# Performance work log

Hardware: AMD Instinct MI355X
Metric: run time of the kernel (lower is better)

Reference implementation:

```python
import jax, jax.numpy as jnp
import numpy as np

B, D, E = 128, 1024, 1024   # batch, word_rnn_size, word_encoding_size
NV, NL = 36, 20             # visual regions, language memory slots
T = 4                       # max_att_step
EPS = 0.01                  # opt.epsilon
SCALE = 0.02


def _lstm_cell(x, h, c, Wih, Whh, bih, bhh):
    # torch.nn.LSTMCell gate order: i, f, g, o
    g = x @ Wih.T + bih + h @ Whh.T + bhh
    i, f, gg, o = jnp.split(g, 4, axis=-1)
    c2 = jax.nn.sigmoid(f) * c + jax.nn.sigmoid(i) * jnp.tanh(gg)
    h2 = jax.nn.sigmoid(o) * jnp.tanh(c2)
    return h2, c2


def _kv_attention(h_att, vkey, vval, lkey, lval, kvs):
    # stand-in for the externally-passed kv_attention module:
    # scaled dot-product attention over visual and language memories
    q = h_att + kvs                                   # [B,D]
    inv = 1.0 / np.sqrt(D)
    va = jax.nn.softmax(jnp.einsum('bnd,bd->bn', vkey, q) * inv, axis=-1)
    vctx = jnp.einsum('bn,bnd->bd', va, vval)
    la = jax.nn.softmax(jnp.einsum('bmd,bd->bm', lkey, q) * inv, axis=-1)
    lctx = jnp.einsum('bm,bmd->bd', la, lval)
    return vctx, lctx, jnp.tanh(kvs + vctx + lctx)


def _update_kv(out, vkey, lkey):
    # stand-in for the externally-passed update_kv module
    return vkey + 0.01 * out[:, None, :], lkey + 0.01 * out[:, None, :]


def _forward(xt, fc_feats, visual_value, visual_key, lang_value, lang_key,
             kv_state, state_h, state_c,
             att_Wih, att_Whh, att_bih, att_bhh,
             lang_Wih, lang_Whh, lang_bih, lang_bhh,
             conf_W1, conf_b1, conf_W2, conf_b2,
             it, max_att_step):
    word_exist = (it > 0).astype(jnp.float32)         # [B]
    prev_h = state_h[-1]
    # att_lstm input is constant across halting steps (state is not updated in the loop)
    att_in = jnp.concatenate([prev_h, fc_feats, xt], axis=1)  # [B, E+2D]
    z1 = jnp.zeros((B, 1), jnp.float32)
    zD = jnp.zeros((B, D), jnp.float32)
    zB = jnp.zeros((B,), jnp.float32)
    carry0 = (z1, jnp.ones((B, 1), jnp.float32), zD, zD, zD, zD, zD, zB,
              visual_key, lang_key, kv_state)

    def body(carry, i):
        accum, sel, hA, cA, hL, cL, outA, cost, vkey, lkey, kvs = carry
        h_att, c_att = _lstm_cell(att_in, state_h[0], state_c[0],
                                  att_Wih, att_Whh, att_bih, att_bhh)
        vctx, lctx, kvs = _kv_attention(h_att, vkey, visual_value, lkey, lang_value, kvs)
        lang_in = jnp.concatenate([vctx, lctx, h_att], axis=1)  # [B,3D]
        h_lang, c_lang = _lstm_cell(lang_in, state_h[1], state_c[1],
                                    lang_Wih, lang_Whh, lang_bih, lang_bhh)
        out = h_lang  # F.dropout in eval mode is identity
        vkey, lkey = _update_kv(out, vkey, lkey)
        # confidence MLP: Linear -> ReLU -> Linear -> Sigmoid
        p = jax.nn.sigmoid(jax.nn.relu(h_lang @ conf_W1.T + conf_b1) @ conf_W2.T + conf_b2)  # [B,1]
        beta = p * (1.0 - accum)
        accum = accum + beta * sel
        hA = hA + beta * h_att * sel
        cA = cA + beta * c_att * sel
        hL = hL + beta * h_lang * sel
        cL = cL + beta * c_lang * sel
        outA = outA + beta * out * sel
        cost = cost + (i + 1.0) * (1.0 - p[:, 0]) * sel[:, 0]
        sel = jax.lax.stop_gradient((accum < 1.0 - EPS).astype(jnp.float32)) * sel
        return (accum, sel, hA, cA, hL, cL, outA, cost, vkey, lkey, kvs), None

    carry, _ = jax.lax.scan(body, carry0, jnp.arange(max_att_step, dtype=jnp.float32))
    accum, sel, hA, cA, hL, cL, outA, cost, vkey, lkey, kvs = carry
    hA = hA / accum
    cA = cA / accum
    hL = hL / accum
    cL = cL / accum
    outA = outA / accum
    new_h = jnp.stack([hA, hL])
    new_c = jnp.stack([cA, cL])
    return outA, vkey, lkey, cost * word_exist, new_h, new_c, kvs


def setup_inputs() -> dict:
    ks = jax.random.split(jax.random.key(0), 20)
    n = lambda k, s, sc=1.0: jax.random.normal(k, s, dtype=jnp.float32) * sc
    return {
        'xt': n(ks[0], (B, E)),
        'it': jax.random.randint(ks[1], (B,), 0, 9487, dtype=jnp.int32),
        'fc_feats': n(ks[2], (B, D)),
        'visual_value': n(ks[3], (B, NV, D)),
        'visual_key': n(ks[4], (B, NV, D)),
        'lang_value': n(ks[5], (B, NL, D)),
        'lang_key': n(ks[6], (B, NL, D)),
        'kv_state': n(ks[7], (B, D)),
        'state_h': n(ks[8], (2, B, D)),
        'state_c': n(ks[9], (2, B, D)),
        'max_att_step': T,
        'att_Wih': n(ks[10], (4 * D, E + 2 * D), SCALE),
        'att_Whh': n(ks[11], (4 * D, D), SCALE),
        'att_bih': jnp.zeros((4 * D,), jnp.float32),
        'att_bhh': jnp.zeros((4 * D,), jnp.float32),
        'lang_Wih': n(ks[12], (4 * D, 3 * D), SCALE),
        'lang_Whh': n(ks[13], (4 * D, D), SCALE),
        'lang_bih': jnp.zeros((4 * D,), jnp.float32),
        'lang_bhh': jnp.zeros((4 * D,), jnp.float32),
        'conf_W1': n(ks[14], (D, D), SCALE),
        'conf_b1': jnp.zeros((D,), jnp.float32),
        'conf_W2': n(ks[15], (1, D), SCALE),
        'conf_b2': jnp.zeros((1,), jnp.float32),
    }


def reference(xt, it, fc_feats, visual_value, visual_key, lang_value, lang_key,
              kv_state, state_h, state_c, max_att_step,
              att_Wih, att_Whh, att_bih, att_bhh,
              lang_Wih, lang_Whh, lang_bih, lang_bhh,
              conf_W1, conf_b1, conf_W2, conf_b2):
    return _forward(xt, fc_feats, visual_value, visual_key, lang_value, lang_key,
                    kv_state, state_h, state_c,
                    att_Wih, att_Whh, att_bih, att_bhh,
                    lang_Wih, lang_Whh, lang_bih, lang_bhh,
                    conf_W1, conf_b1, conf_W2, conf_b2,
                    it, max_att_step)
```

## Files before the change

### kernel.cpp

```cpp
#include <hip/hip_runtime.h>
#include <hip/hip_bf16.h>

constexpr int B  = 128;
constexpr int D  = 1024;
constexpr int NV = 36;
constexpr int NL = 20;
constexpr int BD = B * D;
constexpr float EPS = 0.01f;
constexpr int NSLOT = 16;

constexpr long SL  = 524288;
constexpr long SLB = 2097152;
constexpr long SLC = 524288;
constexpr long OFF_GPA   = 0;
constexpr long OFF_GPLB  = OFF_GPA + 16 * SL;
constexpr long OFF_LBASE = OFF_GPLB + 8 * SL;
constexpr long OFF_GPB   = OFF_LBASE + SL;
constexpr long OFF_GPC   = OFF_GPB + 4 * SLB;
constexpr long OFF_HATT2 = OFF_GPC + 4 * SLC;
constexpr long OFF_HLB   = OFF_HATT2 + BD;
constexpr long OFF_CLB   = OFF_HLB + 524288;
constexpr long OFF_S2    = OFF_CLB + 524288;
constexpr long OFF_VVB   = OFF_S2 + BD;
constexpr long OFF_LVB   = OFF_VVB + 2359296;
constexpr long OFF_VKB   = OFF_LVB + 1310720;
constexpr long OFF_LKB   = OFF_VKB + 2359296;
constexpr long OFF_HATB  = OFF_LKB + 1310720;
constexpr long OFF_SH1B  = OFF_HATB + 65536;
constexpr long OFF_VCXB  = OFF_SH1B + 65536;
constexpr long OFF_LCXB  = OFF_VCXB + 262144;

typedef float f32x4 __attribute__((ext_vector_type(4)));
typedef short s16x8 __attribute__((ext_vector_type(8)));

__device__ __forceinline__ float sigf(float x) { return 1.f / (1.f + expf(-x)); }

__device__ __forceinline__ short f2bf(float f) {
  __hip_bfloat16 h = __float2bfloat16(f);
  return *reinterpret_cast<short*>(&h);
}
__device__ __forceinline__ float bf2f(short s) {
  unsigned u = ((unsigned)(unsigned short)s) << 16;
  return __uint_as_float(u);
}

__device__ __forceinline__ f32x4 LD4(const float* p) { return *(const f32x4*)p; }
__device__ __forceinline__ void ST4(float* p, f32x4 v) { *(f32x4*)p = v; }

__device__ __forceinline__ void conv_bf16(const float* __restrict__ src,
                                          __hip_bfloat16* __restrict__ dst,
                                          long nelem) {
  const long total = nelem >> 2;
  for (long i = (long)blockIdx.x * 256 + threadIdx.x; i < total;
       i += (long)gridDim.x * 256) {
    f32x4 v = LD4(src + i * 4);
    *(short4*)((short*)dst + i * 4) =
        short4{f2bf(v[0]), f2bf(v[1]), f2bf(v[2]), f2bf(v[3])};
  }
}

__global__ __launch_bounds__(256) void conv_kv(
    const float* __restrict__ vkey, const float* __restrict__ lkey,
    const float* __restrict__ vval, const float* __restrict__ lval,
    const float* __restrict__ sh1,
    __hip_bfloat16* __restrict__ vkb, __hip_bfloat16* __restrict__ lkb,
    __hip_bfloat16* __restrict__ vvb, __hip_bfloat16* __restrict__ lvb,
    __hip_bfloat16* __restrict__ sh1b) {
  conv_bf16(vkey, vkb, (long)B * NV * 1024);
  conv_bf16(lkey, lkb, (long)B * NL * 1024);
  conv_bf16(vval, vvb, (long)B * NV * 1024);
  conv_bf16(lval, lvb, (long)B * NL * 1024);
  conv_bf16(sh1, sh1b, (long)BD);
}

struct GemmArgs {
  const void* A[NSLOT];
  const float* W[NSLOT];
  long wstride[NSLOT];
  int abf16[NSLOT];
  int klen;
};

__global__ __launch_bounds__(512, 4) void gemm_mfma(GemmArgs ga, int N,
                                                    long pstride,
                                                    float* __restrict__ gpart) {
  __shared__ __align__(16) short As[2][128][72];
  __shared__ __align__(16) short Bs[2][128][72];
  const int z = blockIdx.z;
  const int ab = ga.abf16[z];
  const float* __restrict__ Af = (const float*)ga.A[z];
  const short* __restrict__ Ah = (const short*)ga.A[z];
  const float* __restrict__ W = ga.W[z];
  const long wstr = ga.wstride[z];
  const int brow = blockIdx.y * 128;
  const int bcol = blockIdx.x * 128;
  float* __restrict__ out = gpart + (long)z * pstride;

  const int tid = threadIdx.x;
  const int wave = tid >> 6, lane = tid & 63;
  const int wr = wave >> 2, wc = wave & 3;
  const int lrow = lane & 15;
  const int lk8  = (lane >> 4) * 8;

  f32x4 acc[4][2];
#pragma unroll
  for (int m = 0; m < 4; ++m)
#pragma unroll
    for (int n = 0; n < 2; ++n) acc[m][n] = (f32x4){0.f, 0.f, 0.f, 0.f};

  float4 ra[4], rw[4];
  s16x8 rab[2];
#define LOAD_TILE(KT)                                                          \
  {                                                                            \
    const int kb = (KT) * 64;                                                  \
    if (ab) {                                                                  \
      _Pragma("unroll") for (int i = 0; i < 2; ++i) {                          \
        const int idx = tid + i * 512;                                         \
        const int r = idx >> 3, c8 = (idx & 7) * 8;                            \
        rab[i] = *(const s16x8*)(Ah + (long)(brow + r) * 1024 + kb + c8);      \
      }                                                                        \
    } else {                                                                   \
      _Pragma("unroll") for (int i = 0; i < 4; ++i) {                          \
        const int idx = tid + i * 512;                                         \
        const int r = idx >> 4, c4 = (idx & 15) * 4;                           \
        ra[i] = *(const float4*)(Af + (long)(brow + r) * 1024 + kb + c4);      \
      }                                                                        \
    }                                                                          \
    _Pragma("unroll") for (int i = 0; i < 4; ++i) {                            \
      const int idx = tid + i * 512;                                           \
      const int r = idx >> 4, c4 = (idx & 15) * 4;                             \
      rw[i] = *(const float4*)(W + (long)(bcol + r) * wstr + kb + c4);         \
    }                                                                          \
  }
#define WRITE_TILE(BUF)                                                        \
  {                                                                            \
    if (ab) {                                                                  \
      _Pragma("unroll") for (int i = 0; i < 2; ++i) {                          \
        const int idx = tid + i * 512;                                         \
        const int r = idx >> 3, c8 = (idx & 7) * 8;                            \
        *(s16x8*)(&As[BUF][r][c8]) = rab[i];                                   \
      }                                                                        \
    } else {                                                                   \
      _Pragma("unroll") for (int i = 0; i < 4; ++i) {                          \
        const int idx = tid + i * 512;                                         \
        const int r = idx >> 4, c4 = (idx & 15) * 4;                           \
        *(short4*)(&As[BUF][r][c4]) =                                          \
            short4{f2bf(ra[i].x), f2bf(ra[i].y), f2bf(ra[i].z), f2bf(ra[i].w)};\
      }                                                                        \
    }                                                                          \
    _Pragma("unroll") for (int i = 0; i < 4; ++i) {                            \
      const int idx = tid + i * 512;                                           \
      const int r = idx >> 4, c4 = (idx & 15) * 4;                             \
      *(short4*)(&Bs[BUF][r][c4]) =                                            \
          short4{f2bf(rw[i].x), f2bf(rw[i].y), f2bf(rw[i].z), f2bf(rw[i].w)};  \
    }                                                                          \
  }

  const int ntiles = ga.klen / 64;
  LOAD_TILE(0);
  WRITE_TILE(0);
  __syncthreads();
  for (int kt = 0; kt < ntiles; ++kt) {
    const int cur = kt & 1;
    const bool more = (kt + 1 < ntiles);
    if (more) LOAD_TILE(kt + 1);
#pragma unroll
    for (int kk = 0; kk < 64; kk += 32) {
      s16x8 af[4], bf[2];
#pragma unroll
      for (int m = 0; m < 4; ++m)
        af[m] = *(const s16x8*)(&As[cur][wr * 64 + m * 16 + lrow][kk + lk8]);
#pragma unroll
      for (int n = 0; n < 2; ++n)
        bf[n] = *(const s16x8*)(&Bs[cur][wc * 32 + n * 16 + lrow][kk + lk8]);
#pragma unroll
      for (int m = 0; m < 4; ++m)
#pragma unroll
        for (int n = 0; n < 2; ++n)
          acc[m][n] = __builtin_amdgcn_mfma_f32_16x16x32_bf16(
              af[m], bf[n], acc[m][n], 0, 0, 0);
    }
    if (more) WRITE_TILE(1 - cur);
    __syncthreads();
  }
#undef LOAD_TILE
#undef WRITE_TILE

#pragma unroll
  for (int m = 0; m < 4; ++m) {
#pragma unroll
    for (int n = 0; n < 2; ++n) {
      const int col = bcol + wc * 32 + n * 16 + lrow;
#pragma unroll
      for (int r = 0; r < 4; ++r) {
        const int row = brow + wr * 64 + m * 16 + (lane >> 4) * 4 + r;
        out[(long)row * N + col] = acc[m][n][r];
      }
    }
  }
}

constexpr long O1 = BD;
constexpr long O2 = O1 + (long)B * NV * D;
constexpr long O3 = O2 + (long)B * NL * D;
constexpr long O4 = O3 + B;
constexpr long O5 = O4 + 2L * BD;
constexpr long O6 = O5 + 2L * BD;
constexpr long O7 = O6 + BD;

__global__ __launch_bounds__(256) void lstm_att(
    const float* __restrict__ gp, const float* __restrict__ bih,
    const float* __restrict__ bhh, const float* __restrict__ c_prev,
    float* __restrict__ h, __hip_bfloat16* __restrict__ hb,
    float* __restrict__ out) {
  long idx = ((long)blockIdx.x * 256 + threadIdx.x) * 4;
  if (idx >= BD) return;
  int b = (int)(idx >> 10), d = (int)(idx & 1023);
  const long base = (long)b * 4096 + d;
  f32x4 g[4];
#pragma unroll
  for (int gi = 0; gi < 4; ++gi) {
    const long o = base + gi * 1024;
    f32x4 v = LD4(bih + gi * 1024 + d) + LD4(bhh + gi * 1024 + d);
#pragma unroll
    for (int s = 0; s < 16; ++s) v += LD4(gp + s * SL + o);
    g[gi] = v;
  }
  f32x4 cp = LD4(c_prev + idx), cc, hh;
#pragma unroll
  for (int j = 0; j < 4; ++j) {
    float ccj = sigf(g[1][j]) * cp[j] + sigf(g[0][j]) * tanhf(g[2][j]);
    cc[j] = ccj;
    hh[j] = sigf(g[3][j]) * tanhf(ccj);
  }
  ST4(h + idx, hh);
  *(short4*)((short*)hb + idx) =
      short4{f2bf(hh[0]), f2bf(hh[1]), f2bf(hh[2]), f2bf(hh[3])};
  ST4(out + O4 + idx, hh);
  ST4(out + O5 + idx, cc);
}

__global__ __launch_bounds__(256) void reduce8(
    const float* __restrict__ gp, const float* __restrict__ bih,
    const float* __restrict__ bhh, float* __restrict__ out) {
  long idx = ((long)blockIdx.x * 256 + threadIdx.x) * 4;
  if (idx >= (long)B * 4096) return;
  int col = (int)(idx & 4095);
  f32x4 v = LD4(bih + col) + LD4(bhh + col);
#pragma unroll
  for (int s = 0; s < 8; ++s) v += LD4(gp + s * SL + idx);
  ST4(out + idx, v);
}

__global__ __launch_bounds__(1024) void attn_mega(
    const float* __restrict__ h_att, const float* __restrict__ kv0,
    const __hip_bfloat16* __restrict__ vkb, const __hip_bfloat16* __restrict__ lkb,
    const __hip_bfloat16* __restrict__ vvb, const __hip_bfloat16* __restrict__ lvb,
    __hip_bfloat16* __restrict__ vctxB, __hip_bfloat16* __restrict__ lctxB,
    float* __restrict__ out_kvs) {
  const int b = blockIdx.x, tid = threadIdx.x;
  __shared__ short K[56][1024];
  __shared__ float q[1024];
  __shared__ float wgt[64];
  const int wave = tid >> 6, lane = tid & 63;

  for (int i = tid; i < 56 * 128; i += 1024) {
    const int r = i >> 7, c8 = (i & 127) * 8;
    const __hip_bfloat16* kp = (r < NV)
        ? vkb + ((long)b * NV + r) * 1024
        : lkb + ((long)b * NL + (r - NV)) * 1024;
    *(s16x8*)(&K[r][c8]) = *(const s16x8*)(kp + c8);
  }

  const float ha = h_att[(long)b * 1024 + tid];
  float kv = kv0[(long)b * 1024 + tid];

  for (int step = 0; step < 4; ++step) {
    q[tid] = ha + kv;
    __syncthreads();
    for (int n = wave; n < NV + NL; n += 16) {
      float s = 0.f;
#pragma unroll
      for (int j = 0; j < 2; ++j) {
        const int base = lane * 8 + j * 512;
        s16x8 k8 = *(const s16x8*)(&K[n][base]);
        f32x4 q0 = *(const f32x4*)(&q[base]);
        f32x4 q1 = *(const f32x4*)(&q[base + 4]);
#pragma unroll
        for (int e = 0; e < 4; ++e) {
          s += bf2f(k8[e]) * q0[e];
          s += bf2f(k8[e + 4]) * q1[e];
        }
      }
      for (int m = 32; m >= 1; m >>= 1) s += __shfl_xor(s, m);
      if (lane == 0) wgt[n] = s * (1.0f / 32.0f);
    }
    __syncthreads();
    if (wave == 0) {
      float x = (lane < NV) ? wgt[lane] : -1e30f;
      float m = x;
      for (int k = 32; k >= 1; k >>= 1) m = fmaxf(m, __shfl_xor(m, k));
      float e = (lane < NV) ? expf(x - m) : 0.f;
      float ssum = e;
      for (int k = 32; k >= 1; k >>= 1) ssum += __shfl_xor(ssum, k);
      if (lane < NV) wgt[lane] = e / ssum;
    } else if (wave == 1) {
      float x = (lane < NL) ? wgt[NV + lane] : -1e30f;
      float m = x;
      for (int k = 32; k >= 1; k >>= 1) m = fmaxf(m, __shfl_xor(m, k));
      float e = (lane < NL) ? expf(x - m) : 0.f;
      float ssum = e;
      for (int k = 32; k >= 1; k >>= 1) ssum += __shfl_xor(ssum, k);
      if (lane < NL) wgt[NV + lane] = e / ssum;
    }
    __syncthreads();
    const __hip_bfloat16* vb = vvb + (long)b * NV * 1024 + tid;
    float a0 = 0.f, a1 = 0.f, a2 = 0.f, a3 = 0.f;
#pragma unroll
    for (int n = 0; n < NV; n += 4) {
      a0 += __bfloat162float(vb[(long)(n + 0) * 1024]) * wgt[n + 0];
      a1 += __bfloat162float(vb[(long)(n + 1) * 1024]) * wgt[n + 1];
      a2 += __bfloat162float(vb[(long)(n + 2) * 1024]) * wgt[n + 2];
      a3 += __bfloat162float(vb[(long)(n + 3) * 1024]) * wgt[n + 3];
    }
    const float vc = (a0 + a1) + (a2 + a3);
    const __hip_bfloat16* lb = lvb + (long)b * NL * 1024 + tid;
    float c0 = 0.f, c1 = 0.f, c2 = 0.f, c3 = 0.f;
#pragma unroll
    for (int n = 0; n < NL; n += 4) {
      c0 += __bfloat162float(lb[(long)(n + 0) * 1024]) * wgt[NV + n + 0];
      c1 += __bfloat162float(lb[(long)(n + 1) * 1024]) * wgt[NV + n + 1];
      c2 += __bfloat162float(lb[(long)(n + 2) * 1024]) * wgt[NV + n + 2];
      c3 += __bfloat162float(lb[(long)(n + 3) * 1024]) * wgt[NV + n + 3];
    }
    const float lc = (c0 + c1) + (c2 + c3);
    const long orow = ((long)step * 128 + b) * 1024 + tid;
    vctxB[orow] = __float2bfloat16(vc);
    lctxB[orow] = __float2bfloat16(lc);
    kv = tanhf(kv + vc + lc);
    __syncthreads();
  }
  out_kvs[(long)b * 1024 + tid] = kv;
}

__global__ __launch_bounds__(256) void lstm_batch(
    const float* __restrict__ gpB, const float* __restrict__ lbase,
    const float* __restrict__ sc1, float* __restrict__ hB,
    float* __restrict__ cB) {
  long idx = ((long)blockIdx.x * 256 + threadIdx.x) * 4;
  if (idx >= 512L * 1024) return;
  const int row = (int)(idx >> 10);
  const int b = row & 127;
  const int d = (int)(idx & 1023);
  const long base = (long)row * 4096 + d;
  const long lbbase = (long)b * 4096 + d;
  f32x4 g[4];
#pragma unroll
  for (int gi = 0; gi < 4; ++gi) {
    const long o = gi * 1024;
    f32x4 v = LD4(lbase + lbbase + o);
#pragma unroll
    for (int s = 0; s < 4; ++s) v += LD4(gpB + s * SLB + base + o);
    g[gi] = v;
  }
  f32x4 cp = LD4(sc1 + (long)b * 1024 + d), cc, hh;
#pragma unroll
  for (int j = 0; j < 4; ++j) {
    float ccj = sigf(g[1][j]) * cp[j] + sigf(g[0][j]) * tanhf(g[2][j]);
    cc[j] = ccj;
    hh[j] = sigf(g[3][j]) * tanhf(ccj);
  }
  ST4(cB + idx, cc);
  ST4(hB + idx, hh);
}

__global__ __launch_bounds__(256) void halt_scan(
    const float* __restrict__ gpc, const float* __restrict__ cb1,
    const float* __restrict__ W2, const float* __restrict__ b2,
    const float* __restrict__ hB, const float* __restrict__ cB,
    const int* __restrict__ it, float* __restrict__ Sout,
    float* __restrict__ out) {
  const int b = blockIdx.x, tid = threadIdx.x;
  const int d0 = tid * 4;
  __shared__ float red[256];
  __shared__ float p_sh;
  const f32x4 w4 = LD4(W2 + d0);
  const f32x4 cb = LD4(cb1 + d0);
  f32x4 hl_acc = (f32x4){0.f, 0.f, 0.f, 0.f}, cl_acc = hl_acc, s_acc = hl_acc;
  float a = 0.f, sel = 1.f, cost = 0.f;

  for (int i = 0; i < 4; ++i) {
    const long o = ((long)i * 128 + b) * 1024 + d0;
    f32x4 rv = cb;
#pragma unroll
    for (int s = 0; s < 4; ++s) rv += LD4(gpc + s * SLC + o);
    float part = 0.f;
#pragma unroll
    for (int j = 0; j < 4; ++j) part += fmaxf(rv[j], 0.f) * w4[j];
    red[tid] = part;
    __syncthreads();
    for (int s = 128; s > 0; s >>= 1) {
      if (tid < s) red[tid] += red[tid + s];
      __syncthreads();
    }
    if (tid == 0) p_sh = sigf(red[0] + b2[0]);
    __syncthreads();
    const float p = p_sh;
    const float bs = p * (1.f - a) * sel;
    f32x4 hl = LD4(hB + o), cl = LD4(cB + o);
    hl_acc += hl * bs;
    cl_acc += cl * bs;
    s_acc += hl;
    cost += (float)(i + 1) * (1.f - p) * sel;
    a += bs;
    sel = (a < 1.f - EPS) ? sel : 0.f;
    __syncthreads();
  }
  const float inv_a = 1.f / a;
  const long ob = (long)b * 1024 + d0;
  ST4(out + ob, hl_acc * inv_a);
  ST4(out + O4 + BD + ob, hl_acc * inv_a);
  ST4(out + O5 + BD + ob, cl_acc * inv_a);
  ST4(Sout + ob, s_acc);
  if (tid == 0) out[O3 + b] = cost * ((it[b] > 0) ? 1.f : 0.f);
}

constexpr long VK = (long)B * NV * D;
constexpr long LK = (long)B * NL * D;

__global__ __launch_bounds__(256) void finalize2(
    const __hip_bfloat16* __restrict__ vkb, const __hip_bfloat16* __restrict__ lkb,
    const float* __restrict__ S, float* __restrict__ out) {
  long idx = ((long)blockIdx.x * 256 + threadIdx.x) * 8;
  if (idx < VK) {
    int b = (int)(idx / (NV * 1024));
    int d = (int)(idx & 1023);
    s16x8 k8 = *(const s16x8*)((const short*)vkb + idx);
    f32x4 s0 = LD4(S + (long)b * 1024 + d), s1 = LD4(S + (long)b * 1024 + d + 4);
    f32x4 o0, o1;
#pragma unroll
    for (int j = 0; j < 4; ++j) {
      o0[j] = bf2f(k8[j]) + 0.01f * s0[j];
      o1[j] = bf2f(k8[j + 4]) + 0.01f * s1[j];
    }
    ST4(out + O1 + idx, o0);
    ST4(out + O1 + idx + 4, o1);
  } else if (idx < VK + LK) {
    long r = idx - VK;
    int b = (int)(r / (NL * 1024));
    int d = (int)(r & 1023);
    s16x8 k8 = *(const s16x8*)((const short*)lkb + r);
    f32x4 s0 = LD4(S + (long)b * 1024 + d), s1 = LD4(S + (long)b * 1024 + d + 4);
    f32x4 o0, o1;
#pragma unroll
    for (int j = 0; j < 4; ++j) {
      o0[j] = bf2f(k8[j]) + 0.01f * s0[j];
      o1[j] = bf2f(k8[j + 4]) + 0.01f * s1[j];
    }
    ST4(out + O2 + r, o0);
    ST4(out + O2 + r + 4, o1);
  }
}

extern "C" void kernel_launch(void* const* d_in, const int* in_sizes, int n_in,
                              void* d_out, int out_size, void* d_ws, size_t ws_size,
                              hipStream_t stream) {
  const float* xt   = (const float*)d_in[0];
  const int*   it   = (const int*)d_in[1];
  const float* fc   = (const float*)d_in[2];
  const float* vval = (const float*)d_in[3];
  const float* vkey = (const float*)d_in[4];
  const float* lval = (const float*)d_in[5];
  const float* lkey = (const float*)d_in[6];
  const float* kv0  = (const float*)d_in[7];
  const float* sh   = (const float*)d_in[8];
  const float* sc   = (const float*)d_in[9];
  const float* aWih = (const float*)d_in[11];
  const float* aWhh = (const float*)d_in[12];
  const float* abih = (const float*)d_in[13];
  const float* abhh = (const float*)d_in[14];
  const float* lWih = (const float*)d_in[15];
  const float* lWhh = (const float*)d_in[16];
  const float* lbih = (const float*)d_in[17];
  const float* lbhh = (const float*)d_in[18];
  const float* cW1  = (const float*)d_in[19];
  const float* cb1  = (const float*)d_in[20];
  const float* cW2  = (const float*)d_in[21];
  const float* cb2  = (const float*)d_in[22];

  float* ws = (float*)d_ws;
  float* gpA   = ws + OFF_GPA;
  float* gpLB  = ws + OFF_GPLB;
  float* lbase = ws + OFF_LBASE;
  float* gpB   = ws + OFF_GPB;
  float* gpC   = ws + OFF_GPC;
  float* h_att = ws + OFF_HATT2;
  float* hB    = ws + OFF_HLB;
  float* cB    = ws + OFF_CLB;
  float* Sbuf  = ws + OFF_S2;
  __hip_bfloat16* vvb  = (__hip_bfloat16*)(ws + OFF_VVB);
  __hip_bfloat16* lvb  = (__hip_bfloat16*)(ws + OFF_LVB);
  __hip_bfloat16* vkb  = (__hip_bfloat16*)(ws + OFF_VKB);
  __hip_bfloat16* lkb  = (__hip_bfloat16*)(ws + OFF_LKB);
  __hip_bfloat16* hatb = (__hip_bfloat16*)(ws + OFF_HATB);
  __hip_bfloat16* sh1b = (__hip_bfloat16*)(ws + OFF_SH1B);
  __hip_bfloat16* vcxb = (__hip_bfloat16*)(ws + OFF_VCXB);
  __hip_bfloat16* lcxb = (__hip_bfloat16*)(ws + OFF_LCXB);

  const float* sh1 = sh + BD;
  const float* sc0 = sc;
  const float* sc1 = sc + BD;
  float* out = (float*)d_out;

  conv_kv<<<2048, 256, 0, stream>>>(vkey, lkey, vval, lval, sh1,
                                    vkb, lkb, vvb, lvb, sh1b);

  {
    GemmArgs ga = {};
    const float* Aops[4] = {sh1, fc, xt, sh};
    const float* Wops[4] = {aWih, aWih + 1024, aWih + 2048, aWhh};
    const long wstrs[4] = {3072, 3072, 3072, 1024};
    for (int p = 0; p < 4; ++p)
      for (int q = 0; q < 4; ++q) {
        ga.A[p * 4 + q] = Aops[p] + q * 256;
        ga.W[p * 4 + q] = Wops[p] + q * 256;
        ga.wstride[p * 4 + q] = wstrs[p];
      }
    ga.klen = 256;
    gemm_mfma<<<dim3(32, 1, 16), 512, 0, stream>>>(ga, 4096, SL, gpA);
  }
  lstm_att<<<128, 256, 0, stream>>>(gpA, abih, abhh, sc0, h_att, hatb, out);

  attn_mega<<<128, 1024, 0, stream>>>(h_att, kv0, vkb, lkb, vvb, lvb,
                                      vcxb, lcxb, out + O6);

  {
    GemmArgs ga = {};
    for (int q = 0; q < 4; ++q) {
      ga.A[q] = (const void*)((const short*)sh1b + q * 256);
      ga.W[q] = lWhh + q * 256;
      ga.wstride[q] = 1024;
      ga.abf16[q] = 1;
      ga.A[4 + q] = (const void*)((const short*)hatb + q * 256);
      ga.W[4 + q] = lWih + 2048 + q * 256;
      ga.wstride[4 + q] = 3072;
      ga.abf16[4 + q] = 1;
    }
    ga.klen = 256;
    gemm_mfma<<<dim3(32, 1, 8), 512, 0, stream>>>(ga, 4096, SL, gpLB);
  }
  reduce8<<<512, 256, 0, stream>>>(gpLB, lbih, lbhh, lbase);

  {
    GemmArgs ga = {};
    ga.A[0] = vcxb;                              ga.W[0] = lWih;
    ga.wstride[0] = 3072; ga.abf16[0] = 1;
    ga.A[1] = (const void*)((const short*)vcxb + 512); ga.W[1] = lWih + 512;
    ga.wstride[1] = 3072; ga.abf16[1] = 1;
    ga.A[2] = lcxb;                              ga.W[2] = lWih + 1024;
    ga.wstride[2] = 3072; ga.abf16[2] = 1;
    ga.A[3] = (const void*)((const short*)lcxb + 512); ga.W[3] = lWih + 1536;
    ga.wstride[3] = 3072; ga.abf16[3] = 1;
    ga.klen = 512;
    gemm_mfma<<<dim3(32, 4, 4), 512, 0, stream>>>(ga, 4096, SLB, gpB);
  }
  lstm_batch<<<512, 256, 0, stream>>>(gpB, lbase, sc1, hB, cB);

  {
    GemmArgs ga = {};
    for (int q = 0; q < 4; ++q) {
      ga.A[q] = hB + q * 256;
      ga.W[q] = cW1 + q * 256;
      ga.wstride[q] = 1024;
    }
    ga.klen = 256;
    gemm_mfma<<<dim3(8, 4, 4), 512, 0, stream>>>(ga, 1024, SLC, gpC);
  }
  halt_scan<<<128, 256, 0, stream>>>(gpC, cb1, cW2, cb2, hB, cB, it,
                                     Sbuf, out);
  finalize2<<<3584, 256, 0, stream>>>(vkb, lkb, Sbuf, out);
}
```

Baseline: 156.3 us.

## Fuse independent kernels into heterogeneous launches to overlap work and cut launches

Merges pairs of independent stages into single launches whose blocks branch on block index. The bf16 conversion runs alongside the first GEMM, attention alongside the language-hidden GEMM, the bias reduction alongside the context GEMM, and the key-update finalize alongside the confidence GEMM. The finalize now recomputes the per-batch sum of hidden states itself instead of reading a buffer written by the halting scan. Attention is reshaped to 512 threads reading keys straight from global memory instead of staging them in LDS. This cuts launch count and fills idle CUs, at the cost of mixed-workload blocks sharing the GEMM's launch bounds and LDS footprint, and uncached key reads in attention.

Result: slower. 184.5 us (+18.0%).

```diff
diff --git a/kernel.cpp b/kernel.cpp
--- a/kernel.cpp
+++ b/kernel.cpp
@@ -20,8 +20,7 @@
 constexpr long OFF_HATT2 = OFF_GPC + 4 * SLC;
 constexpr long OFF_HLB   = OFF_HATT2 + BD;
 constexpr long OFF_CLB   = OFF_HLB + 524288;
-constexpr long OFF_S2    = OFF_CLB + 524288;
-constexpr long OFF_VVB   = OFF_S2 + BD;
+constexpr long OFF_VVB   = OFF_CLB + 524288;
 constexpr long OFF_LVB   = OFF_VVB + 2359296;
 constexpr long OFF_VKB   = OFF_LVB + 1310720;
 constexpr long OFF_LKB   = OFF_VKB + 2359296;
@@ -32,6 +31,7 @@
 
 typedef float f32x4 __attribute__((ext_vector_type(4)));
 typedef short s16x8 __attribute__((ext_vector_type(8)));
+typedef short ldsT[128][72];
 
 __device__ __forceinline__ float sigf(float x) { return 1.f / (1.f + expf(-x)); }
 
@@ -47,31 +47,15 @@
 __device__ __forceinline__ f32x4 LD4(const float* p) { return *(const f32x4*)p; }
 __device__ __forceinline__ void ST4(float* p, f32x4 v) { *(f32x4*)p = v; }
 
-__device__ __forceinline__ void conv_bf16(const float* __restrict__ src,
-                                          __hip_bfloat16* __restrict__ dst,
-                                          long nelem) {
-  const long total = nelem >> 2;
-  for (long i = (long)blockIdx.x * 256 + threadIdx.x; i < total;
-       i += (long)gridDim.x * 256) {
-    f32x4 v = LD4(src + i * 4);
-    *(short4*)((short*)dst + i * 4) =
-        short4{f2bf(v[0]), f2bf(v[1]), f2bf(v[2]), f2bf(v[3])};
-  }
-}
-
-__global__ __launch_bounds__(256) void conv_kv(
-    const float* __restrict__ vkey, const float* __restrict__ lkey,
-    const float* __restrict__ vval, const float* __restrict__ lval,
-    const float* __restrict__ sh1,
-    __hip_bfloat16* __restrict__ vkb, __hip_bfloat16* __restrict__ lkb,
-    __hip_bfloat16* __restrict__ vvb, __hip_bfloat16* __restrict__ lvb,
-    __hip_bfloat16* __restrict__ sh1b) {
-  conv_bf16(vkey, vkb, (long)B * NV * 1024);
-  conv_bf16(lkey, lkb, (long)B * NL * 1024);
-  conv_bf16(vval, vvb, (long)B * NV * 1024);
-  conv_bf16(lval, lvb, (long)B * NL * 1024);
-  conv_bf16(sh1, sh1b, (long)BD);
-}
+constexpr long O1 = BD;
+constexpr long O2 = O1 + (long)B * NV * D;
+constexpr long O3 = O2 + (long)B * NL * D;
+constexpr long O4 = O3 + B;
+constexpr long O5 = O4 + 2L * BD;
+constexpr long O6 = O5 + 2L * BD;
+constexpr long O7 = O6 + BD;
+constexpr long VK = (long)B * NV * D;
+constexpr long LK = (long)B * NL * D;
 
 struct GemmArgs {
   const void* A[NSLOT];
@@ -81,19 +65,19 @@
   int klen;
 };
 
-__global__ __launch_bounds__(512, 4) void gemm_mfma(GemmArgs ga, int N,
-                                                    long pstride,
-                                                    float* __restrict__ gpart) {
-  __shared__ __align__(16) short As[2][128][72];
-  __shared__ __align__(16) short Bs[2][128][72];
-  const int z = blockIdx.z;
+__device__ __forceinline__ void gemm_body(const GemmArgs& ga, int N,
+                                          long pstride,
+                                          float* __restrict__ gpart,
+                                          int bx, int by, int bz,
+                                          ldsT* As, ldsT* Bs) {
+  const int z = bz;
   const int ab = ga.abf16[z];
   const float* __restrict__ Af = (const float*)ga.A[z];
   const short* __restrict__ Ah = (const short*)ga.A[z];
   const float* __restrict__ W = ga.W[z];
   const long wstr = ga.wstride[z];
-  const int brow = blockIdx.y * 128;
-  const int bcol = blockIdx.x * 128;
+  const int brow = by * 128;
+  const int bcol = bx * 128;
   float* __restrict__ out = gpart + (long)z * pstride;
 
   const int tid = threadIdx.x;
@@ -200,13 +184,38 @@
   }
 }
 
-constexpr long O1 = BD;
-constexpr long O2 = O1 + (long)B * NV * D;
-constexpr long O3 = O2 + (long)B * NL * D;
-constexpr long O4 = O3 + B;
-constexpr long O5 = O4 + 2L * BD;
-constexpr long O6 = O5 + 2L * BD;
-constexpr long O7 = O6 + BD;
+__device__ __forceinline__ void conv_b(const float* __restrict__ src,
+                                       __hip_bfloat16* __restrict__ dst,
+                                       long nelem, int bid, int nb) {
+  const long total = nelem >> 2;
+  for (long i = (long)bid * 512 + threadIdx.x; i < total; i += (long)nb * 512) {
+    f32x4 v = LD4(src + i * 4);
+    *(short4*)((short*)dst + i * 4) =
+        short4{f2bf(v[0]), f2bf(v[1]), f2bf(v[2]), f2bf(v[3])};
+  }
+}
+
+__global__ __launch_bounds__(512, 4) void fusedA(
+    GemmArgs ga, float* __restrict__ gpA,
+    const float* __restrict__ vkey, const float* __restrict__ lkey,
+    const float* __restrict__ vval, const float* __restrict__ lval,
+    const float* __restrict__ sh1,
+    __hip_bfloat16* __restrict__ vkb, __hip_bfloat16* __restrict__ lkb,
+    __hip_bfloat16* __restrict__ vvb, __hip_bfloat16* __restrict__ lvb,
+    __hip_bfloat16* __restrict__ sh1b) {
+  __shared__ __align__(16) union { struct { ldsT As[2]; ldsT Bs[2]; } g; } sm;
+  const int bid = blockIdx.x;
+  if (bid < 256) {
+    conv_b(vkey, vkb, (long)B * NV * 1024, bid, 256);
+    conv_b(lkey, lkb, (long)B * NL * 1024, bid, 256);
+    conv_b(vval, vvb, (long)B * NV * 1024, bid, 256);
+    conv_b(lval, lvb, (long)B * NL * 1024, bid, 256);
+    conv_b(sh1, sh1b, (long)BD, bid, 256);
+  } else {
+    const int g = bid - 256;
+    gemm_body(ga, 4096, SL, gpA, g & 31, 0, g >> 5, sm.g.As, sm.g.Bs);
+  }
+}
 
 __global__ __launch_bounds__(256) void lstm_att(
     const float* __restrict__ gp, const float* __restrict__ bih,
@@ -240,50 +249,33 @@
   ST4(out + O5 + idx, cc);
 }
 
-__global__ __launch_bounds__(256) void reduce8(
-    const float* __restrict__ gp, const float* __restrict__ bih,
-    const float* __restrict__ bhh, float* __restrict__ out) {
-  long idx = ((long)blockIdx.x * 256 + threadIdx.x) * 4;
-  if (idx >= (long)B * 4096) return;
-  int col = (int)(idx & 4095);
-  f32x4 v = LD4(bih + col) + LD4(bhh + col);
-#pragma unroll
-  for (int s = 0; s < 8; ++s) v += LD4(gp + s * SL + idx);
-  ST4(out + idx, v);
-}
-
-__global__ __launch_bounds__(1024) void attn_mega(
-    const float* __restrict__ h_att, const float* __restrict__ kv0,
+__device__ __forceinline__ void attn_body(
+    int b, const float* __restrict__ h_att, const float* __restrict__ kv0,
     const __hip_bfloat16* __restrict__ vkb, const __hip_bfloat16* __restrict__ lkb,
     const __hip_bfloat16* __restrict__ vvb, const __hip_bfloat16* __restrict__ lvb,
     __hip_bfloat16* __restrict__ vctxB, __hip_bfloat16* __restrict__ lctxB,
-    float* __restrict__ out_kvs) {
-  const int b = blockIdx.x, tid = threadIdx.x;
-  __shared__ short K[56][1024];
-  __shared__ float q[1024];
-  __shared__ float wgt[64];
+    float* __restrict__ out_kvs, float* q, float* wgt) {
+  const int tid = threadIdx.x;
   const int wave = tid >> 6, lane = tid & 63;
-
-  for (int i = tid; i < 56 * 128; i += 1024) {
-    const int r = i >> 7, c8 = (i & 127) * 8;
-    const __hip_bfloat16* kp = (r < NV)
-        ? vkb + ((long)b * NV + r) * 1024
-        : lkb + ((long)b * NL + (r - NV)) * 1024;
-    *(s16x8*)(&K[r][c8]) = *(const s16x8*)(kp + c8);
-  }
-
-  const float ha = h_att[(long)b * 1024 + tid];
-  float kv = kv0[(long)b * 1024 + tid];
+  const int d0 = tid, d1 = tid + 512;
+  const float ha0 = h_att[(long)b * 1024 + d0];
+  const float ha1 = h_att[(long)b * 1024 + d1];
+  float kva = kv0[(long)b * 1024 + d0];
+  float kvc = kv0[(long)b * 1024 + d1];
 
   for (int step = 0; step < 4; ++step) {
-    q[tid] = ha + kv;
-    __syncthreads();
-    for (int n = wave; n < NV + NL; n += 16) {
+    q[d0] = ha0 + kva;
+    q[d1] = ha1 + kvc;
+    __syncthreads();
+    for (int n = wave; n < NV + NL; n += 8) {
+      const short* kp = (n < NV)
+          ? (const short*)vkb + ((long)b * NV + n) * 1024
+          : (const short*)lkb + ((long)b * NL + (n - NV)) * 1024;
       float s = 0.f;
 #pragma unroll
       for (int j = 0; j < 2; ++j) {
         const int base = lane * 8 + j * 512;
-        s16x8 k8 = *(const s16x8*)(&K[n][base]);
+        s16x8 k8 = *(const s16x8*)(kp + base);
         f32x4 q0 = *(const f32x4*)(&q[base]);
         f32x4 q1 = *(const f32x4*)(&q[base + 4]);
 #pragma unroll
@@ -314,33 +306,80 @@
       if (lane < NL) wgt[NV + lane] = e / ssum;
     }
     __syncthreads();
-    const __hip_bfloat16* vb = vvb + (long)b * NV * 1024 + tid;
-    float a0 = 0.f, a1 = 0.f, a2 = 0.f, a3 = 0.f;
-#pragma unroll
-    for (int n = 0; n < NV; n += 4) {
-      a0 += __bfloat162float(vb[(long)(n + 0) * 1024]) * wgt[n + 0];
-      a1 += __bfloat162float(vb[(long)(n + 1) * 1024]) * wgt[n + 1];
-      a2 += __bfloat162float(vb[(long)(n + 2) * 1024]) * wgt[n + 2];
-      a3 += __bfloat162float(vb[(long)(n + 3) * 1024]) * wgt[n + 3];
-    }
-    const float vc = (a0 + a1) + (a2 + a3);
-    const __hip_bfloat16* lb = lvb + (long)b * NL * 1024 + tid;
-    float c0 = 0.f, c1 = 0.f, c2 = 0.f, c3 = 0.f;
-#pragma unroll
-    for (int n = 0; n < NL; n += 4) {
-      c0 += __bfloat162float(lb[(long)(n + 0) * 1024]) * wgt[NV + n + 0];
-      c1 += __bfloat162float(lb[(long)(n + 1) * 1024]) * wgt[NV + n + 1];
-      c2 += __bfloat162float(lb[(long)(n + 2) * 1024]) * wgt[NV + n + 2];
-      c3 += __bfloat162float(lb[(long)(n + 3) * 1024]) * wgt[NV + n + 3];
-    }
-    const float lc = (c0 + c1) + (c2 + c3);
-    const long orow = ((long)step * 128 + b) * 1024 + tid;
-    vctxB[orow] = __float2bfloat16(vc);
-    lctxB[orow] = __float2bfloat16(lc);
-    kv = tanhf(kv + vc + lc);
-    __syncthreads();
-  }
-  out_kvs[(long)b * 1024 + tid] = kv;
+    const short* vb = (const short*)vvb + (long)b * NV * 1024;
+    float v00 = 0.f, v01 = 0.f, v10 = 0.f, v11 = 0.f;
+#pragma unroll
+    for (int n = 0; n < NV; n += 2) {
+      v00 += bf2f(vb[(long)(n + 0) * 1024 + d0]) * wgt[n + 0];
+      v10 += bf2f(vb[(long)(n + 0) * 1024 + d1]) * wgt[n + 0];
+      v01 += bf2f(vb[(long)(n + 1) * 1024 + d0]) * wgt[n + 1];
+      v11 += bf2f(vb[(long)(n + 1) * 1024 + d1]) * wgt[n + 1];
+    }
+    const float vc0 = v00 + v01, vc1 = v10 + v11;
+    const short* lb = (const short*)lvb + (long)b * NL * 1024;
+    float l00 = 0.f, l01 = 0.f, l10 = 0.f, l11 = 0.f;
+#pragma unroll
+    for (int n = 0; n < NL; n += 2) {
+      l00 += bf2f(lb[(long)(n + 0) * 1024 + d0]) * wgt[NV + n + 0];
+      l10 += bf2f(lb[(long)(n + 0) * 1024 + d1]) * wgt[NV + n + 0];
+      l01 += bf2f(lb[(long)(n + 1) * 1024 + d0]) * wgt[NV + n + 1];
+      l11 += bf2f(lb[(long)(n + 1) * 1024 + d1]) * wgt[NV + n + 1];
+    }
+    const float lc0 = l00 + l01, lc1 = l10 + l11;
+    const long orow = ((long)step * 128 + b) * 1024;
+    vctxB[orow + d0] = __float2bfloat16(vc0);
+    vctxB[orow + d1] = __float2bfloat16(vc1);
+    lctxB[orow + d0] = __float2bfloat16(lc0);
+    lctxB[orow + d1] = __float2bfloat16(lc1);
+    kva = tanhf(kva + vc0 + lc0);
+    kvc = tanhf(kvc + vc1 + lc1);
+    __syncthreads();
+  }
+  out_kvs[(long)b * 1024 + d0] = kva;
+  out_kvs[(long)b * 1024 + d1] = kvc;
+}
+
+__global__ __launch_bounds__(512, 4) void fusedB(
+    GemmArgs ga, float* __restrict__ gpLB,
+    const float* __restrict__ h_att, const float* __restrict__ kv0,
+    const __hip_bfloat16* __restrict__ vkb, const __hip_bfloat16* __restrict__ lkb,
+    const __hip_bfloat16* __restrict__ vvb, const __hip_bfloat16* __restrict__ lvb,
+    __hip_bfloat16* __restrict__ vctxB, __hip_bfloat16* __restrict__ lctxB,
+    float* __restrict__ out_kvs) {
+  __shared__ __align__(16) union {
+    struct { ldsT As[2]; ldsT Bs[2]; } g;
+    struct { float q[1024]; float wgt[64]; } a;
+  } sm;
+  const int bid = blockIdx.x;
+  if (bid < 128) {
+    attn_body(bid, h_att, kv0, vkb, lkb, vvb, lvb, vctxB, lctxB, out_kvs,
+              sm.a.q, sm.a.wgt);
+  } else {
+    const int g = bid - 128;
+    gemm_body(ga, 4096, SL, gpLB, g & 31, 0, g >> 5, sm.g.As, sm.g.Bs);
+  }
+}
+
+__global__ __launch_bounds__(512, 4) void fusedD(
+    GemmArgs ga, float* __restrict__ gpB,
+    const float* __restrict__ gpLB, const float* __restrict__ lbih,
+    const float* __restrict__ lbhh, float* __restrict__ lbase) {
+  __shared__ __align__(16) union { struct { ldsT As[2]; ldsT Bs[2]; } g; } sm;
+  const int bid = blockIdx.x;
+  if (bid < 128) {
+    const long total = (long)B * 4096 / 4;
+    for (long i = (long)bid * 512 + threadIdx.x; i < total; i += 128L * 512) {
+      const long idx = i * 4;
+      const int col = (int)(idx & 4095);
+      f32x4 v = LD4(lbih + col) + LD4(lbhh + col);
+#pragma unroll
+      for (int s = 0; s < 8; ++s) v += LD4(gpLB + s * SL + idx);
+      ST4(lbase + idx, v);
+    }
+  } else {
+    const int g = bid - 128;
+    gemm_body(ga, 4096, SLB, gpB, g & 31, (g >> 5) & 3, g >> 7, sm.g.As, sm.g.Bs);
+  }
 }
 
 __global__ __launch_bounds__(256) void lstm_batch(
@@ -374,19 +413,71 @@
   ST4(hB + idx, hh);
 }
 
+__global__ __launch_bounds__(512, 4) void fusedC(
+    GemmArgs ga, float* __restrict__ gpC, const float* __restrict__ hB,
+    const __hip_bfloat16* __restrict__ vkb, const __hip_bfloat16* __restrict__ lkb,
+    float* __restrict__ out) {
+  __shared__ __align__(16) union {
+    struct { ldsT As[2]; ldsT Bs[2]; } g;
+    struct { float Ssh[1024]; } f;
+  } sm;
+  const int bid = blockIdx.x;
+  if (bid < 128) {
+    gemm_body(ga, 1024, SLC, gpC, bid & 7, (bid >> 3) & 3, bid >> 5,
+              sm.g.As, sm.g.Bs);
+    return;
+  }
+  const int fb = bid - 128;
+  const long base = (long)fb * 4096;
+  const bool isV = (base < VK);
+  const int b = isV ? (int)(base / (NV * 1024))
+                    : (int)((base - VK) / (NL * 1024));
+  const int tid = threadIdx.x;
+  for (int d = tid; d < 1024; d += 512) {
+    float s = 0.f;
+#pragma unroll
+    for (int st = 0; st < 4; ++st) s += hB[((long)st * 128 + b) * 1024 + d];
+    sm.f.Ssh[d] = s;
+  }
+  __syncthreads();
+  const long idx = base + (long)tid * 8;
+  const int d = (int)(idx & 1023);
+  if (isV) {
+    s16x8 k8 = *(const s16x8*)((const short*)vkb + idx);
+    f32x4 o0, o1;
+#pragma unroll
+    for (int j = 0; j < 4; ++j) {
+      o0[j] = bf2f(k8[j]) + 0.01f * sm.f.Ssh[d + j];
+      o1[j] = bf2f(k8[j + 4]) + 0.01f * sm.f.Ssh[d + 4 + j];
+    }
+    ST4(out + O1 + idx, o0);
+    ST4(out + O1 + idx + 4, o1);
+  } else {
+    const long r = idx - VK;
+    s16x8 k8 = *(const s16x8*)((const short*)lkb + r);
+    f32x4 o0, o1;
+#pragma unroll
+    for (int j = 0; j < 4; ++j) {
+      o0[j] = bf2f(k8[j]) + 0.01f * sm.f.Ssh[d + j];
+      o1[j] = bf2f(k8[j + 4]) + 0.01f * sm.f.Ssh[d + 4 + j];
+    }
+    ST4(out + O2 + r, o0);
+    ST4(out + O2 + r + 4, o1);
+  }
+}
+
 __global__ __launch_bounds__(256) void halt_scan(
     const float* __restrict__ gpc, const float* __restrict__ cb1,
     const float* __restrict__ W2, const float* __restrict__ b2,
     const float* __restrict__ hB, const float* __restrict__ cB,
-    const int* __restrict__ it, float* __restrict__ Sout,
-    float* __restrict__ out) {
+    const int* __restrict__ it, float* __restrict__ out) {
   const int b = blockIdx.x, tid = threadIdx.x;
   const int d0 = tid * 4;
   __shared__ float red[256];
   __shared__ float p_sh;
   const f32x4 w4 = LD4(W2 + d0);
   const f32x4 cb = LD4(cb1 + d0);
-  f32x4 hl_acc = (f32x4){0.f, 0.f, 0.f, 0.f}, cl_acc = hl_acc, s_acc = hl_acc;
+  f32x4 hl_acc = (f32x4){0.f, 0.f, 0.f, 0.f}, cl_acc = hl_acc;
   float a = 0.f, sel = 1.f, cost = 0.f;
 
   for (int i = 0; i < 4; ++i) {
@@ -410,7 +501,6 @@
     f32x4 hl = LD4(hB + o), cl = LD4(cB + o);
     hl_acc += hl * bs;
     cl_acc += cl * bs;
-    s_acc += hl;
     cost += (float)(i + 1) * (1.f - p) * sel;
     a += bs;
     sel = (a < 1.f - EPS) ? sel : 0.f;
@@ -421,45 +511,7 @@
   ST4(out + ob, hl_acc * inv_a);
   ST4(out + O4 + BD + ob, hl_acc * inv_a);
   ST4(out + O5 + BD + ob, cl_acc * inv_a);
-  ST4(Sout + ob, s_acc);
   if (tid == 0) out[O3 + b] = cost * ((it[b] > 0) ? 1.f : 0.f);
-}
-
-constexpr long VK = (long)B * NV * D;
-constexpr long LK = (long)B * NL * D;
-
-__global__ __launch_bounds__(256) void finalize2(
-    const __hip_bfloat16* __restrict__ vkb, const __hip_bfloat16* __restrict__ lkb,
-    const float* __restrict__ S, float* __restrict__ out) {
-  long idx = ((long)blockIdx.x * 256 + threadIdx.x) * 8;
-  if (idx < VK) {
-    int b = (int)(idx / (NV * 1024));
-    int d = (int)(idx & 1023);
-    s16x8 k8 = *(const s16x8*)((const short*)vkb + idx);
-    f32x4 s0 = LD4(S + (long)b * 1024 + d), s1 = LD4(S + (long)b * 1024 + d + 4);
-    f32x4 o0, o1;
-#pragma unroll
-    for (int j = 0; j < 4; ++j) {
-      o0[j] = bf2f(k8[j]) + 0.01f * s0[j];
-      o1[j] = bf2f(k8[j + 4]) + 0.01f * s1[j];
-    }
-    ST4(out + O1 + idx, o0);
-    ST4(out + O1 + idx + 4, o1);
-  } else if (idx < VK + LK) {
-    long r = idx - VK;
-    int b = (int)(r / (NL * 1024));
-    int d = (int)(r & 1023);
-    s16x8 k8 = *(const s16x8*)((const short*)lkb + r);
-    f32x4 s0 = LD4(S + (long)b * 1024 + d), s1 = LD4(S + (long)b * 1024 + d + 4);
-    f32x4 o0, o1;
-#pragma unroll
-    for (int j = 0; j < 4; ++j) {
-      o0[j] = bf2f(k8[j]) + 0.01f * s0[j];
-      o1[j] = bf2f(k8[j + 4]) + 0.01f * s1[j];
-    }
-    ST4(out + O2 + r, o0);
-    ST4(out + O2 + r + 4, o1);
-  }
 }
 
 extern "C" void kernel_launch(void* const* d_in, const int* in_sizes, int n_in,
@@ -497,7 +549,6 @@
   float* h_att = ws + OFF_HATT2;
   float* hB    = ws + OFF_HLB;
   float* cB    = ws + OFF_CLB;
-  float* Sbuf  = ws + OFF_S2;
   __hip_bfloat16* vvb  = (__hip_bfloat16*)(ws + OFF_VVB);
   __hip_bfloat16* lvb  = (__hip_bfloat16*)(ws + OFF_LVB);
   __hip_bfloat16* vkb  = (__hip_bfloat16*)(ws + OFF_VKB);
@@ -511,9 +562,6 @@
   const float* sc0 = sc;
   const float* sc1 = sc + BD;
   float* out = (float*)d_out;
-
-  conv_kv<<<2048, 256, 0, stream>>>(vkey, lkey, vval, lval, sh1,
-                                    vkb, lkb, vvb, lvb, sh1b);
 
   {
     GemmArgs ga = {};
@@ -527,12 +575,10 @@
         ga.wstride[p * 4 + q] = wstrs[p];
       }
     ga.klen = 256;
-    gemm_mfma<<<dim3(32, 1, 16), 512, 0, stream>>>(ga, 4096, SL, gpA);
+    fusedA<<<768, 512, 0, stream>>>(ga, gpA, vkey, lkey, vval, lval, sh1,
+                                    vkb, lkb, vvb, lvb, sh1b);
   }
   lstm_att<<<128, 256, 0, stream>>>(gpA, abih, abhh, sc0, h_att, hatb, out);
-
-  attn_mega<<<128, 1024, 0, stream>>>(h_att, kv0, vkb, lkb, vvb, lvb,
-                                      vcxb, lcxb, out + O6);
 
   {
     GemmArgs ga = {};
@@ -547,10 +593,9 @@
       ga.abf16[4 + q] = 1;
     }
     ga.klen = 256;
-    gemm_mfma<<<dim3(32, 1, 8), 512, 0, stream>>>(ga, 4096, SL, gpLB);
-  }
-  reduce8<<<512, 256, 0, stream>>>(gpLB, lbih, lbhh, lbase);
-
+    fusedB<<<384, 512, 0, stream>>>(ga, gpLB, h_att, kv0, vkb, lkb, vvb, lvb,
+                                    vcxb, lcxb, out + O6);
+  }
   {
     GemmArgs ga = {};
     ga.A[0] = vcxb;                              ga.W[0] = lWih;
@@ -562,7 +607,7 @@
     ga.A[3] = (const void*)((const short*)lcxb + 512); ga.W[3] = lWih + 1536;
     ga.wstride[3] = 3072; ga.abf16[3] = 1;
     ga.klen = 512;
-    gemm_mfma<<<dim3(32, 4, 4), 512, 0, stream>>>(ga, 4096, SLB, gpB);
+    fusedD<<<640, 512, 0, stream>>>(ga, gpB, gpLB, lbih, lbhh, lbase);
   }
   lstm_batch<<<512, 256, 0, stream>>>(gpB, lbase, sc1, hB, cB);
 
@@ -574,9 +619,7 @@
       ga.wstride[q] = 1024;
     }
     ga.klen = 256;
-    gemm_mfma<<<dim3(8, 4, 4), 512, 0, stream>>>(ga, 1024, SLC, gpC);
-  }
-  halt_scan<<<128, 256, 0, stream>>>(gpC, cb1, cW2, cb2, hB, cB, it,
-                                     Sbuf, out);
-  finalize2<<<3584, 256, 0, stream>>>(vkb, lkb, Sbuf, out);
-}
+    fusedC<<<1920, 512, 0, stream>>>(ga, gpC, hB, vkb, lkb, out);
+  }
+  halt_scan<<<128, 256, 0, stream>>>(gpC, cb1, cW2, cb2, hB, cB, it, out);
+}
```
